# Optimization experiments

Hardware: AMD Instinct MI355X
Metric: run time of the kernel (lower is better)

The kernel has to match this reference:

```python
import jax, jax.numpy as jnp
import numpy as np

B, M = 512, 32          # graphs, atoms per graph
N = B * M               # 16384 nodes
F_IN, H, L = 16, 128, 2 # input feat, hidden, n interaction layers
CUTOFF = 1.0
BOX = 2.0               # side of position box -> avg degree ~16 at r=1


def _glorot(k, shape):
    fan_in = shape[-2]
    return jax.random.normal(k, shape, dtype=jnp.float32) / np.sqrt(fan_in)


def setup_inputs():
    key = jax.random.key(0)
    ks = jax.random.split(key, 12)
    return {
        "h": jax.random.normal(ks[0], (N, F_IN), dtype=jnp.float32),
        "x": jax.random.uniform(ks[1], (N, 3), dtype=jnp.float32) * BOX,
        "batch": jnp.repeat(jnp.arange(B, dtype=jnp.int32), M),
        "W_in": _glorot(ks[2], (F_IN, H)), "b_in": jnp.zeros((H,), jnp.float32),
        "We1": _glorot(ks[3], (L, 2 * H + 1, H)), "be1": jnp.zeros((L, H), jnp.float32),
        "We2": _glorot(ks[4], (L, H, H)), "be2": jnp.zeros((L, H), jnp.float32),
        "Wh1": _glorot(ks[5], (L, 2 * H, H)), "bh1": jnp.zeros((L, H), jnp.float32),
        "Wh2": _glorot(ks[6], (L, H, H)), "bh2": jnp.zeros((L, H), jnp.float32),
        "W_out": _glorot(ks[7], (H, H)), "b_out": jnp.zeros((H,), jnp.float32),
        "Wn1": _glorot(ks[8], (H, H)), "bn1": jnp.zeros((H,), jnp.float32),
        "Wn2": _glorot(ks[9], (H, 1)), "bn2": jnp.zeros((1,), jnp.float32),
    }


def reference(h, x, batch, W_in, b_in, We1, be1, We2, be2, Wh1, bh1, Wh2, bh2, W_out, b_out, Wn1, bn1, Wn2, bn2):
    # radius graph within each molecule, fixed-shape dense mask [B,M,M]
    xg = x.reshape(B, M, 3)
    diff = xg[:, :, None, :] - xg[:, None, :, :]                 # [B,M,M,3]
    d2 = jnp.sum(diff * diff, axis=-1)                            # [B,M,M]
    adj = (d2 < CUTOFF * CUTOFF) & (~jnp.eye(M, dtype=bool))      # no self-loops

    hg = (h @ W_in + b_in).reshape(B, M, H)                       # embedding_in
    for l in range(L):  # sake_conv interaction layers
        Wa, Wb, wd = We1[l, :H], We1[l, H:2 * H], We1[l, 2 * H]
        mi = jnp.einsum('bmh,hk->bmk', hg, Wa)
        mj = jnp.einsum('bmh,hk->bmk', hg, Wb)
        # edge message phi_e([h_i, h_j, ||x_i-x_j||^2])
        m = jax.nn.silu(mi[:, :, None, :] + mj[:, None, :, :] + d2[..., None] * wd + be1[l])
        m = jax.nn.silu(jnp.einsum('bijh,hk->bijk', m, We2[l]) + be2[l])
        m = jnp.where(adj[..., None], m, 0.0)
        agg = jnp.sum(m, axis=2)                                  # scatter-add over neighbors j
        # node update phi_h([h_i, m_i]) with residual
        u = jax.nn.silu(jnp.einsum('bmh,hk->bmk', hg, Wh1[l, :H])
                        + jnp.einsum('bmh,hk->bmk', agg, Wh1[l, H:]) + bh1[l])
        hg = hg + jnp.einsum('bmh,hk->bmk', u, Wh2[l]) + bh2[l]

    ho = hg.reshape(N, H) @ W_out + b_out                         # embedding_out
    e = jax.nn.silu(ho @ Wn1 + bn1) @ Wn2 + bn2                   # energy_network -> [N,1]
    out = jax.ops.segment_sum(e, batch, num_segments=B)           # per-graph energy pooling
    return out.squeeze()
```

## Files before the change

kernel.cpp:

```cpp
#include <hip/hip_runtime.h>
#include <hip/hip_bf16.h>


#define NB 512

typedef __bf16 bf16x8 __attribute__((ext_vector_type(8)));
typedef __bf16 bf16x2 __attribute__((ext_vector_type(2)));
typedef float f32x4 __attribute__((ext_vector_type(4)));

__device__ __forceinline__ unsigned short f2bf(float f) {
    unsigned int u = __float_as_uint(f);
    u = u + 0x7FFFu + ((u >> 16) & 1u);
    return (unsigned short)(u >> 16);
}
__device__ __forceinline__ unsigned int packbf(float lo, float hi) {
    bf16x2 t;
    t.x = (__bf16)lo;
    t.y = (__bf16)hi;
    return __builtin_bit_cast(unsigned int, t);
}
__device__ __forceinline__ float bflo(unsigned int u) { return __uint_as_float(u << 16); }
__device__ __forceinline__ float bfhi(unsigned int u) { return __uint_as_float(u & 0xffff0000u); }
__device__ __forceinline__ float bf2f(unsigned short u) { return __uint_as_float((unsigned int)u << 16); }
__device__ __forceinline__ float silu_f(float v) {
    return v * __builtin_amdgcn_rcpf(1.0f + __expf(-v));
}

__global__ __launch_bounds__(256) void prep_weights(
        const float* __restrict__ We1, const float* __restrict__ We2,
        const float* __restrict__ Wh1, const float* __restrict__ Wh2,
        const float* __restrict__ W_out, const float* __restrict__ Wn1,
        unsigned short* __restrict__ ws) {
    __shared__ unsigned short t[32][33];
    const int mtx  = blockIdx.x >> 4;
    const int tile = blockIdx.x & 15;
    const int kt = tile >> 2, nt = tile & 3;
    const int tx = threadIdx.x & 31, ty = threadIdx.x >> 5;

    const int l    = (mtx < 12) ? (mtx / 6) : 0;
    const int kind = (mtx < 12) ? (mtx % 6) : (6 + (mtx - 12));
    const float* src = nullptr;
    switch (kind) {
        case 0: src = We1 + (size_t)(l*257      )*128; break;
        case 1: src = We1 + (size_t)(l*257 + 128)*128; break;
        case 2: src = We2 + (size_t)(l*128      )*128; break;
        case 3: src = Wh1 + (size_t)(l*256      )*128; break;
        case 4: src = Wh1 + (size_t)(l*256 + 128)*128; break;
        case 5: src = Wh2 + (size_t)(l*128      )*128; break;
        case 6: src = W_out; break;
        case 7: src = Wn1;  break;
    }
    #pragma unroll
    for (int r = 0; r < 4; r++) {
        int k = kt*32 + ty + r*8;
        int n = nt*32 + tx;
        t[tx][ty + r*8] = f2bf(src[(size_t)k*128 + n]);
    }
    __syncthreads();
    unsigned short* dst = ws + ((size_t)mtx << 14);
    #pragma unroll
    for (int r = 0; r < 4; r++) {
        int nl = ty + r*8;
        int n = nt*32 + nl, k = kt*32 + tx;
        dst[(size_t)n*128 + k] = t[nl][tx];
    }
}

#define MFMA16(ACC, A, B) (ACC) = __builtin_amdgcn_mfma_f32_16x16x32_bf16((A), (B), (ACC), 0, 0, 0)

__global__ __launch_bounds__(256, 2) void sake_kernel(
    const float* __restrict__ h,   const float* __restrict__ x,
    const float* __restrict__ W_in,const float* __restrict__ b_in,
    const float* __restrict__ We1, const float* __restrict__ be1,
    const float* __restrict__ be2, const float* __restrict__ bh1,
    const float* __restrict__ bh2, const float* __restrict__ b_out,
    const float* __restrict__ bn1, const float* __restrict__ Wn2,
    const float* __restrict__ bn2, const unsigned short* __restrict__ wt,
    float* __restrict__ out)
{
    __shared__ __align__(16) float          s_hg[32*129];
    __shared__ __align__(16) unsigned short s_mimj[32*264];
    __shared__ __align__(16) unsigned short s_A1[32*136];
    __shared__ __align__(16) unsigned short s_A2[32*136];
    __shared__ __align__(16) float          s_nd2[32*16];
    __shared__ __align__(16) float          s_wd[128];
    __shared__ __align__(16) unsigned short s_be2[128];
    __shared__ __align__(16) unsigned char  s_nbr[32][16];
    __shared__ __align__(16) unsigned char  s_cnt[32];

    const int tid  = threadIdx.x;
    const int b    = blockIdx.x;
    const int w    = tid >> 6;
    const int lane = tid & 63;
    const int quad = lane >> 4;
    const int lm   = lane & 15;
    const int mt   = w & 1;
    const int ng   = w >> 1;

    if (tid < 32) {
        const float xx = x[(b*32+tid)*3+0];
        const float xy = x[(b*32+tid)*3+1];
        const float xz = x[(b*32+tid)*3+2];
        int c = 0;
        for (int j = 0; j < 32; j++) {
            float ox = __shfl(xx, j);
            float oy = __shfl(xy, j);
            float oz = __shfl(xz, j);
            float dx = xx - ox, dy = xy - oy, dz = xz - oz;
            float d2 = dx*dx + dy*dy + dz*dz;
            if (d2 < 1.0f && j != tid) {
                if (c < 16) { s_nbr[tid][c] = (unsigned char)j; s_nd2[tid*16 + c] = d2; }
                c++;
            }
        }
        for (int q = c; q < 16; q++) { s_nbr[tid][q] = (unsigned char)tid; s_nd2[tid*16 + q] = 0.0f; }
        s_cnt[tid] = (unsigned char)c;
    }
    {
        int k = tid & 127, mg = tid >> 7;
        float c0 = W_in[       k], c1 = W_in[ 128+k], c2 = W_in[ 256+k], c3 = W_in[ 384+k];
        float c4 = W_in[ 512+k], c5 = W_in[ 640+k], c6 = W_in[ 768+k], c7 = W_in[ 896+k];
        float c8 = W_in[1024+k], c9 = W_in[1152+k], c10= W_in[1280+k], c11= W_in[1408+k];
        float c12= W_in[1536+k], c13= W_in[1664+k], c14= W_in[1792+k], c15= W_in[1920+k];
        float bi = b_in[k];
        for (int rr = 0; rr < 16; rr++) {
            int m = mg*16 + rr;
            const float4* h4 = (const float4*)(h + (size_t)(b*32 + m)*16);
            float4 h0 = h4[0], h1 = h4[1], h2 = h4[2], h3 = h4[3];
            float acc = bi
                + h0.x*c0  + h0.y*c1  + h0.z*c2  + h0.w*c3
                + h1.x*c4  + h1.y*c5  + h1.z*c6  + h1.w*c7
                + h2.x*c8  + h2.y*c9  + h2.z*c10 + h2.w*c11
                + h3.x*c12 + h3.y*c13 + h3.z*c14 + h3.w*c15;
            s_hg[m*129 + k] = acc;
        }
    }
    __syncthreads();

    for (int l = 0; l < 2; l++) {
        {
            int m = tid >> 3, c = (tid & 7) * 16;
            const float* hp = &s_hg[m*129 + c];
            uint4 pa, pb;
            pa.x = packbf(hp[0],  hp[1]);  pa.y = packbf(hp[2],  hp[3]);
            pa.z = packbf(hp[4],  hp[5]);  pa.w = packbf(hp[6],  hp[7]);
            pb.x = packbf(hp[8],  hp[9]);  pb.y = packbf(hp[10], hp[11]);
            pb.z = packbf(hp[12], hp[13]); pb.w = packbf(hp[14], hp[15]);
            *(uint4*)&s_A1[m*136 + c]     = pa;
            *(uint4*)&s_A1[m*136 + c + 8] = pb;
        }
        if (tid < 128) {
            s_wd[tid]  = We1[(l*257 + 256)*128 + tid];
            s_be2[tid] = f2bf(be2[l*128 + tid]);
        }
        __syncthreads();

        #pragma unroll 1
        for (int t4 = 0; t4 < 8; t4++) {
            int nt = ng + t4*2;
            const unsigned short* bt = wt + (((size_t)l*6 + (nt < 8 ? 0 : 1)) << 14);
            int ncl = (nt & 7)*16 + lm;
            f32x4 acc = {0.f,0.f,0.f,0.f};
            #pragma unroll
            for (int kb = 0; kb < 4; kb++) {
                bf16x8 a  = *(const bf16x8*)&s_A1[(mt*16+lm)*136 + kb*32 + quad*8];
                bf16x8 bb = *(const bf16x8*)&bt[ncl*128 + kb*32 + quad*8];
                MFMA16(acc, a, bb);
            }
            int c = nt*16 + lm;
            float bias = (nt >= 8) ? be1[l*128 + ncl] : 0.0f;
            s_mimj[(mt*16 + quad*4 + 0)*264 + c] = f2bf(acc.x + bias);
            s_mimj[(mt*16 + quad*4 + 1)*264 + c] = f2bf(acc.y + bias);
            s_mimj[(mt*16 + quad*4 + 2)*264 + c] = f2bf(acc.z + bias);
            s_mimj[(mt*16 + quad*4 + 3)*264 + c] = f2bf(acc.w + bias);
        }
        __syncthreads();

        {
            const unsigned short* we2t = wt + (((size_t)l*6 + 2) << 14);
            const unsigned short* bbase = we2t + lm*128 + quad*8;
            bf16x8 b0 = *(const bf16x8*)(bbase      );
            bf16x8 b1 = *(const bf16x8*)(bbase +  32);
            bf16x8 b2 = *(const bf16x8*)(bbase +  64);
            bf16x8 b3 = *(const bf16x8*)(bbase +  96);
            #pragma unroll 1
            for (int ii = 0; ii < 8; ii++) {
                const int i = ii*4 + w;
                const int cnt = s_cnt[i];
                const uint4 miu0 = *(const uint4*)&s_mimj[i*264 +  0 + quad*8];
                const uint4 miu1 = *(const uint4*)&s_mimj[i*264 + 32 + quad*8];
                const uint4 miu2 = *(const uint4*)&s_mimj[i*264 + 64 + quad*8];
                const uint4 miu3 = *(const uint4*)&s_mimj[i*264 + 96 + quad*8];
#define MAKE_AF(J, KB, MIU, AF) { \
    const uint4 mju = *(const uint4*)&s_mimj[(J)*264 + 128 + (KB)*32 + quad*8]; \
    const float4 wa = *(const float4*)&s_wd[(KB)*32 + quad*8]; \
    const float4 wb = *(const float4*)&s_wd[(KB)*32 + quad*8 + 4]; \
    uint4 au; \
    au.x = packbf(silu_f(bflo(MIU.x)+bflo(mju.x)+d2v*wa.x), silu_f(bfhi(MIU.x)+bfhi(mju.x)+d2v*wa.y)); \
    au.y = packbf(silu_f(bflo(MIU.y)+bflo(mju.y)+d2v*wa.z), silu_f(bfhi(MIU.y)+bfhi(mju.y)+d2v*wa.w)); \
    au.z = packbf(silu_f(bflo(MIU.z)+bflo(mju.z)+d2v*wb.x), silu_f(bfhi(MIU.z)+bfhi(mju.z)+d2v*wb.y)); \
    au.w = packbf(silu_f(bflo(MIU.w)+bflo(mju.w)+d2v*wb.z), silu_f(bfhi(MIU.w)+bfhi(mju.w)+d2v*wb.w)); \
    AF = __builtin_bit_cast(bf16x8, au); }
                if (cnt <= 16) {
                    const int j = s_nbr[i][lm];
                    const float d2v = s_nd2[i*16 + lm];
                    bf16x8 a00, a01, a02, a03;
                    MAKE_AF(j, 0, miu0, a00) MAKE_AF(j, 1, miu1, a01)
                    MAKE_AF(j, 2, miu2, a02) MAKE_AF(j, 3, miu3, a03)
                    const int jb0 = quad*4;
                    const float mk00 = (jb0 + 0 < cnt) ? 1.f : 0.f;
                    const float mk01 = (jb0 + 1 < cnt) ? 1.f : 0.f;
                    const float mk02 = (jb0 + 2 < cnt) ? 1.f : 0.f;
                    const float mk03 = (jb0 + 3 < cnt) ? 1.f : 0.f;
                    #pragma unroll 1
                    for (int nt = 0; nt < 8; nt++) {
                        const unsigned short* np = bbase + (((nt + 1) & 7) * 2048);
                        bf16x8 n0 = *(const bf16x8*)(np      );
                        bf16x8 n1 = *(const bf16x8*)(np +  32);
                        bf16x8 n2 = *(const bf16x8*)(np +  64);
                        bf16x8 n3 = *(const bf16x8*)(np +  96);
                        f32x4 ac0 = {0.f,0.f,0.f,0.f};
                        MFMA16(ac0, a00, b0); MFMA16(ac0, a01, b1);
                        MFMA16(ac0, a02, b2); MFMA16(ac0, a03, b3);
                        const float bv = bf2f(s_be2[nt*16 + lm]);
                        float part = mk00*silu_f(ac0.x + bv) + mk01*silu_f(ac0.y + bv)
                                   + mk02*silu_f(ac0.z + bv) + mk03*silu_f(ac0.w + bv);
                        part += __shfl_xor(part, 16);
                        part += __shfl_xor(part, 32);
                        if (lane < 16) s_A2[i*136 + nt*16 + lane] = f2bf(part);
                        b0 = n0; b1 = n1; b2 = n2; b3 = n3;
                    }
                } else {
                    const float xi0 = x[(b*32+i)*3+0];
                    const float xi1 = x[(b*32+i)*3+1];
                    const float xi2 = x[(b*32+i)*3+2];
                    float da0 = xi0 - x[(b*32+lm)*3+0];
                    float da1 = xi1 - x[(b*32+lm)*3+1];
                    float da2 = xi2 - x[(b*32+lm)*3+2];
                    const float d2a = da0*da0 + da1*da1 + da2*da2;
                    float db0 = xi0 - x[(b*32+16+lm)*3+0];
                    float db1 = xi1 - x[(b*32+16+lm)*3+1];
                    float db2 = xi2 - x[(b*32+16+lm)*3+2];
                    const float d2b = db0*db0 + db1*db1 + db2*db2;
                    const unsigned long long balA = __ballot(d2a < 1.0f && lm != i);
                    const unsigned long long balB = __ballot(d2b < 1.0f && (16+lm) != i);
                    bf16x8 a00, a01, a02, a03;
                    bf16x8 a10, a11, a12, a13;
                    {
                        const int j = lm;
                        const float d2v = d2a;
                        MAKE_AF(j, 0, miu0, a00) MAKE_AF(j, 1, miu1, a01)
                        MAKE_AF(j, 2, miu2, a02) MAKE_AF(j, 3, miu3, a03)
                    }
                    {
                        const int j = 16 + lm;
                        const float d2v = d2b;
                        MAKE_AF(j, 0, miu0, a10) MAKE_AF(j, 1, miu1, a11)
                        MAKE_AF(j, 2, miu2, a12) MAKE_AF(j, 3, miu3, a13)
                    }
                    const int jb0 = quad*4;
                    const float mk00 = ((balA >> (jb0 + 0)) & 1ull) ? 1.f : 0.f;
                    const float mk01 = ((balA >> (jb0 + 1)) & 1ull) ? 1.f : 0.f;
                    const float mk02 = ((balA >> (jb0 + 2)) & 1ull) ? 1.f : 0.f;
                    const float mk03 = ((balA >> (jb0 + 3)) & 1ull) ? 1.f : 0.f;
                    const float mk10 = ((balB >> (jb0 + 0)) & 1ull) ? 1.f : 0.f;
                    const float mk11 = ((balB >> (jb0 + 1)) & 1ull) ? 1.f : 0.f;
                    const float mk12 = ((balB >> (jb0 + 2)) & 1ull) ? 1.f : 0.f;
                    const float mk13 = ((balB >> (jb0 + 3)) & 1ull) ? 1.f : 0.f;
                    #pragma unroll 1
                    for (int nt = 0; nt < 8; nt++) {
                        const unsigned short* np = bbase + (((nt + 1) & 7) * 2048);
                        bf16x8 n0 = *(const bf16x8*)(np      );
                        bf16x8 n1 = *(const bf16x8*)(np +  32);
                        bf16x8 n2 = *(const bf16x8*)(np +  64);
                        bf16x8 n3 = *(const bf16x8*)(np +  96);
                        f32x4 ac0 = {0.f,0.f,0.f,0.f};
                        f32x4 ac1 = {0.f,0.f,0.f,0.f};
                        MFMA16(ac0, a00, b0); MFMA16(ac0, a01, b1);
                        MFMA16(ac0, a02, b2); MFMA16(ac0, a03, b3);
                        MFMA16(ac1, a10, b0); MFMA16(ac1, a11, b1);
                        MFMA16(ac1, a12, b2); MFMA16(ac1, a13, b3);
                        const float bv = bf2f(s_be2[nt*16 + lm]);
                        float part = mk00*silu_f(ac0.x + bv) + mk01*silu_f(ac0.y + bv)
                                   + mk02*silu_f(ac0.z + bv) + mk03*silu_f(ac0.w + bv)
                                   + mk10*silu_f(ac1.x + bv) + mk11*silu_f(ac1.y + bv)
                                   + mk12*silu_f(ac1.z + bv) + mk13*silu_f(ac1.w + bv);
                        part += __shfl_xor(part, 16);
                        part += __shfl_xor(part, 32);
                        if (lane < 16) s_A2[i*136 + nt*16 + lane] = f2bf(part);
                        b0 = n0; b1 = n1; b2 = n2; b3 = n3;
                    }
                }
#undef MAKE_AF
            }
        }
        __syncthreads();

        unsigned short* s_u = s_mimj;
        {
            const unsigned short* w1a = wt + (((size_t)l*6 + 3) << 14);
            const unsigned short* w1b = wt + (((size_t)l*6 + 4) << 14);
#define U_GEMM(T2) { \
    const int nt = ng + (T2)*2, ncl = nt*16 + lm; \
    f32x4 acc = {0.f,0.f,0.f,0.f}; \
    _Pragma("unroll") \
    for (int kb = 0; kb < 4; kb++) { \
        bf16x8 a  = *(const bf16x8*)&s_A1[(mt*16+lm)*136 + kb*32 + quad*8]; \
        bf16x8 bb = *(const bf16x8*)&w1a[ncl*128 + kb*32 + quad*8]; \
        MFMA16(acc, a, bb); } \
    _Pragma("unroll") \
    for (int kb = 0; kb < 4; kb++) { \
        bf16x8 a  = *(const bf16x8*)&s_A2[(mt*16+lm)*136 + kb*32 + quad*8]; \
        bf16x8 bb = *(const bf16x8*)&w1b[ncl*128 + kb*32 + quad*8]; \
        MFMA16(acc, a, bb); } \
    const float bh = bh1[l*128 + ncl]; \
    s_u[(mt*16 + quad*4 + 0)*136 + ncl] = f2bf(silu_f(acc.x + bh)); \
    s_u[(mt*16 + quad*4 + 1)*136 + ncl] = f2bf(silu_f(acc.y + bh)); \
    s_u[(mt*16 + quad*4 + 2)*136 + ncl] = f2bf(silu_f(acc.z + bh)); \
    s_u[(mt*16 + quad*4 + 3)*136 + ncl] = f2bf(silu_f(acc.w + bh)); }
            U_GEMM(0) U_GEMM(1) U_GEMM(2) U_GEMM(3)
#undef U_GEMM
        }
        __syncthreads();

        {
            const unsigned short* w2 = wt + (((size_t)l*6 + 5) << 14);
#define H_GEMM(T2) { \
    const int nt = ng + (T2)*2, ncl = nt*16 + lm; \
    f32x4 acc = {0.f,0.f,0.f,0.f}; \
    _Pragma("unroll") \
    for (int kb = 0; kb < 4; kb++) { \
        bf16x8 a  = *(const bf16x8*)&s_u[(mt*16+lm)*136 + kb*32 + quad*8]; \
        bf16x8 bb = *(const bf16x8*)&w2[ncl*128 + kb*32 + quad*8]; \
        MFMA16(acc, a, bb); } \
    const float bh = bh2[l*128 + ncl]; \
    s_hg[(mt*16 + quad*4 + 0)*129 + ncl] += acc.x + bh; \
    s_hg[(mt*16 + quad*4 + 1)*129 + ncl] += acc.y + bh; \
    s_hg[(mt*16 + quad*4 + 2)*129 + ncl] += acc.z + bh; \
    s_hg[(mt*16 + quad*4 + 3)*129 + ncl] += acc.w + bh; }
            H_GEMM(0) H_GEMM(1) H_GEMM(2) H_GEMM(3)
#undef H_GEMM
        }
        __syncthreads();
    }

    {
        int m = tid >> 3, c = (tid & 7) * 16;
        const float* hp = &s_hg[m*129 + c];
        uint4 pa, pb;
        pa.x = packbf(hp[0],  hp[1]);  pa.y = packbf(hp[2],  hp[3]);
        pa.z = packbf(hp[4],  hp[5]);  pa.w = packbf(hp[6],  hp[7]);
        pb.x = packbf(hp[8],  hp[9]);  pb.y = packbf(hp[10], hp[11]);
        pb.z = packbf(hp[12], hp[13]); pb.w = packbf(hp[14], hp[15]);
        *(uint4*)&s_A1[m*136 + c]     = pa;
        *(uint4*)&s_A1[m*136 + c + 8] = pb;
    }
    __syncthreads();
    {
        const unsigned short* wo = wt + ((size_t)12 << 14);
#define O_GEMM(T2) { \
    const int nt = ng + (T2)*2, ncl = nt*16 + lm; \
    f32x4 acc = {0.f,0.f,0.f,0.f}; \
    _Pragma("unroll") \
    for (int kb = 0; kb < 4; kb++) { \
        bf16x8 a  = *(const bf16x8*)&s_A1[(mt*16+lm)*136 + kb*32 + quad*8]; \
        bf16x8 bb = *(const bf16x8*)&wo[ncl*128 + kb*32 + quad*8]; \
        MFMA16(acc, a, bb); } \
    const float bo = b_out[ncl]; \
    s_A2[(mt*16 + quad*4 + 0)*136 + ncl] = f2bf(acc.x + bo); \
    s_A2[(mt*16 + quad*4 + 1)*136 + ncl] = f2bf(acc.y + bo); \
    s_A2[(mt*16 + quad*4 + 2)*136 + ncl] = f2bf(acc.z + bo); \
    s_A2[(mt*16 + quad*4 + 3)*136 + ncl] = f2bf(acc.w + bo); }
        O_GEMM(0) O_GEMM(1) O_GEMM(2) O_GEMM(3)
#undef O_GEMM
    }
    __syncthreads();
    float* s_g = (float*)s_mimj;
    {
        const unsigned short* wn1 = wt + ((size_t)13 << 14);
#define G_GEMM(T2) { \
    const int nt = ng + (T2)*2, ncl = nt*16 + lm; \
    f32x4 acc = {0.f,0.f,0.f,0.f}; \
    _Pragma("unroll") \
    for (int kb = 0; kb < 4; kb++) { \
        bf16x8 a  = *(const bf16x8*)&s_A2[(mt*16+lm)*136 + kb*32 + quad*8]; \
        bf16x8 bb = *(const bf16x8*)&wn1[ncl*128 + kb*32 + quad*8]; \
        MFMA16(acc, a, bb); } \
    const float bn = bn1[ncl]; \
    s_g[(mt*16 + quad*4 + 0)*129 + ncl] = silu_f(acc.x + bn); \
    s_g[(mt*16 + quad*4 + 1)*129 + ncl] = silu_f(acc.y + bn); \
    s_g[(mt*16 + quad*4 + 2)*129 + ncl] = silu_f(acc.z + bn); \
    s_g[(mt*16 + quad*4 + 3)*129 + ncl] = silu_f(acc.w + bn); }
        G_GEMM(0) G_GEMM(1) G_GEMM(2) G_GEMM(3)
#undef G_GEMM
    }
    __syncthreads();
    float* s_ep = s_nd2;
    {
        int m = tid >> 3, s = tid & 7;
        float acc = 0.f;
        #pragma unroll
        for (int q = 0; q < 16; q++) {
            int hh = s*16 + q;
            acc += s_g[m*129 + hh] * Wn2[hh];
        }
        s_ep[tid] = acc;
    }
    __syncthreads();
    if (tid < 32) {
        float e = bn2[0];
        #pragma unroll
        for (int s = 0; s < 8; s++) e += s_ep[tid*8 + s];
        #pragma unroll
        for (int off = 16; off >= 1; off >>= 1) e += __shfl_down(e, off, 32);
        if (tid == 0) out[b] = e;
    }
}

extern "C" void kernel_launch(void* const* d_in, const int* in_sizes, int n_in,
                              void* d_out, int out_size, void* d_ws, size_t ws_size,
                              hipStream_t stream) {
    const float* h     = (const float*)d_in[0];
    const float* x     = (const float*)d_in[1];
    const float* W_in  = (const float*)d_in[3];
    const float* b_in  = (const float*)d_in[4];
    const float* We1   = (const float*)d_in[5];
    const float* be1   = (const float*)d_in[6];
    const float* We2   = (const float*)d_in[7];
    const float* be2   = (const float*)d_in[8];
    const float* Wh1   = (const float*)d_in[9];
    const float* bh1   = (const float*)d_in[10];
    const float* Wh2   = (const float*)d_in[11];
    const float* bh2   = (const float*)d_in[12];
    const float* W_out = (const float*)d_in[13];
    const float* b_out = (const float*)d_in[14];
    const float* Wn1   = (const float*)d_in[15];
    const float* bn1   = (const float*)d_in[16];
    const float* Wn2   = (const float*)d_in[17];
    const float* bn2   = (const float*)d_in[18];
    unsigned short* ws = (unsigned short*)d_ws;
    float* outp = (float*)d_out;

    prep_weights<<<14*16, 256, 0, stream>>>(We1, We2, Wh1, Wh2, W_out, Wn1, ws);
    sake_kernel<<<NB, 256, 0, stream>>>(h, x, W_in, b_in, We1, be1, be2, bh1, bh2,
                                        b_out, bn1, Wn2, bn2, ws, outp);
}
```

Measured before the change: 256.9 us.

## Hold full We2 tile in registers and fuse bf16 staging into producer stages

The edge-MLP second GEMM now preloads all eight We2 column tiles (32 bf16x8 vectors) and the be2 bias values into registers once per layer. The nt loop is fully unrolled, so it no longer reloads weights from global memory for every node i. The bf16 copy of hg in s_A1 is now written directly by the embedding and residual-update stages. This removes the separate pack passes and two barriers per layer, and the mi/mj GEMM loop is unrolled by two. The cost is much higher register pressure, which could lower occupancy or cause spills.

Measured after the change: 218.0 us. -15.1%, faster.

```diff
diff --git a/kernel.cpp b/kernel.cpp
--- a/kernel.cpp
+++ b/kernel.cpp
@@ -133,29 +133,18 @@
                 + h2.x*c8  + h2.y*c9  + h2.z*c10 + h2.w*c11
                 + h3.x*c12 + h3.y*c13 + h3.z*c14 + h3.w*c15;
             s_hg[m*129 + k] = acc;
+            s_A1[m*136 + k] = f2bf(acc);
         }
     }
     __syncthreads();
 
     for (int l = 0; l < 2; l++) {
-        {
-            int m = tid >> 3, c = (tid & 7) * 16;
-            const float* hp = &s_hg[m*129 + c];
-            uint4 pa, pb;
-            pa.x = packbf(hp[0],  hp[1]);  pa.y = packbf(hp[2],  hp[3]);
-            pa.z = packbf(hp[4],  hp[5]);  pa.w = packbf(hp[6],  hp[7]);
-            pb.x = packbf(hp[8],  hp[9]);  pb.y = packbf(hp[10], hp[11]);
-            pb.z = packbf(hp[12], hp[13]); pb.w = packbf(hp[14], hp[15]);
-            *(uint4*)&s_A1[m*136 + c]     = pa;
-            *(uint4*)&s_A1[m*136 + c + 8] = pb;
-        }
         if (tid < 128) {
             s_wd[tid]  = We1[(l*257 + 256)*128 + tid];
             s_be2[tid] = f2bf(be2[l*128 + tid]);
         }
-        __syncthreads();
-
-        #pragma unroll 1
+
+        #pragma unroll 2
         for (int t4 = 0; t4 < 8; t4++) {
             int nt = ng + t4*2;
             const unsigned short* bt = wt + (((size_t)l*6 + (nt < 8 ? 0 : 1)) << 14);
@@ -179,10 +168,17 @@
         {
             const unsigned short* we2t = wt + (((size_t)l*6 + 2) << 14);
             const unsigned short* bbase = we2t + lm*128 + quad*8;
-            bf16x8 b0 = *(const bf16x8*)(bbase      );
-            bf16x8 b1 = *(const bf16x8*)(bbase +  32);
-            bf16x8 b2 = *(const bf16x8*)(bbase +  64);
-            bf16x8 b3 = *(const bf16x8*)(bbase +  96);
+            bf16x8 wreg[8][4];
+            #pragma unroll
+            for (int nt = 0; nt < 8; nt++) {
+                #pragma unroll
+                for (int kb = 0; kb < 4; kb++)
+                    wreg[nt][kb] = *(const bf16x8*)(bbase + nt*2048 + kb*32);
+            }
+            float bvv[8];
+            #pragma unroll
+            for (int nt = 0; nt < 8; nt++) bvv[nt] = bf2f(s_be2[nt*16 + lm]);
+
             #pragma unroll 1
             for (int ii = 0; ii < 8; ii++) {
                 const int i = ii*4 + w;
@@ -212,23 +208,17 @@
                     const float mk01 = (jb0 + 1 < cnt) ? 1.f : 0.f;
                     const float mk02 = (jb0 + 2 < cnt) ? 1.f : 0.f;
                     const float mk03 = (jb0 + 3 < cnt) ? 1.f : 0.f;
-                    #pragma unroll 1
+                    #pragma unroll
                     for (int nt = 0; nt < 8; nt++) {
-                        const unsigned short* np = bbase + (((nt + 1) & 7) * 2048);
-                        bf16x8 n0 = *(const bf16x8*)(np      );
-                        bf16x8 n1 = *(const bf16x8*)(np +  32);
-                        bf16x8 n2 = *(const bf16x8*)(np +  64);
-                        bf16x8 n3 = *(const bf16x8*)(np +  96);
                         f32x4 ac0 = {0.f,0.f,0.f,0.f};
-                        MFMA16(ac0, a00, b0); MFMA16(ac0, a01, b1);
-                        MFMA16(ac0, a02, b2); MFMA16(ac0, a03, b3);
-                        const float bv = bf2f(s_be2[nt*16 + lm]);
+                        MFMA16(ac0, a00, wreg[nt][0]); MFMA16(ac0, a01, wreg[nt][1]);
+                        MFMA16(ac0, a02, wreg[nt][2]); MFMA16(ac0, a03, wreg[nt][3]);
+                        const float bv = bvv[nt];
                         float part = mk00*silu_f(ac0.x + bv) + mk01*silu_f(ac0.y + bv)
                                    + mk02*silu_f(ac0.z + bv) + mk03*silu_f(ac0.w + bv);
                         part += __shfl_xor(part, 16);
                         part += __shfl_xor(part, 32);
                         if (lane < 16) s_A2[i*136 + nt*16 + lane] = f2bf(part);
-                        b0 = n0; b1 = n1; b2 = n2; b3 = n3;
                     }
                 } else {
                     const float xi0 = x[(b*32+i)*3+0];
@@ -267,20 +257,15 @@
                     const float mk11 = ((balB >> (jb0 + 1)) & 1ull) ? 1.f : 0.f;
                     const float mk12 = ((balB >> (jb0 + 2)) & 1ull) ? 1.f : 0.f;
                     const float mk13 = ((balB >> (jb0 + 3)) & 1ull) ? 1.f : 0.f;
-                    #pragma unroll 1
+                    #pragma unroll
                     for (int nt = 0; nt < 8; nt++) {
-                        const unsigned short* np = bbase + (((nt + 1) & 7) * 2048);
-                        bf16x8 n0 = *(const bf16x8*)(np      );
-                        bf16x8 n1 = *(const bf16x8*)(np +  32);
-                        bf16x8 n2 = *(const bf16x8*)(np +  64);
-                        bf16x8 n3 = *(const bf16x8*)(np +  96);
                         f32x4 ac0 = {0.f,0.f,0.f,0.f};
                         f32x4 ac1 = {0.f,0.f,0.f,0.f};
-                        MFMA16(ac0, a00, b0); MFMA16(ac0, a01, b1);
-                        MFMA16(ac0, a02, b2); MFMA16(ac0, a03, b3);
-                        MFMA16(ac1, a10, b0); MFMA16(ac1, a11, b1);
-                        MFMA16(ac1, a12, b2); MFMA16(ac1, a13, b3);
-                        const float bv = bf2f(s_be2[nt*16 + lm]);
+                        MFMA16(ac0, a00, wreg[nt][0]); MFMA16(ac0, a01, wreg[nt][1]);
+                        MFMA16(ac0, a02, wreg[nt][2]); MFMA16(ac0, a03, wreg[nt][3]);
+                        MFMA16(ac1, a10, wreg[nt][0]); MFMA16(ac1, a11, wreg[nt][1]);
+                        MFMA16(ac1, a12, wreg[nt][2]); MFMA16(ac1, a13, wreg[nt][3]);
+                        const float bv = bvv[nt];
                         float part = mk00*silu_f(ac0.x + bv) + mk01*silu_f(ac0.y + bv)
                                    + mk02*silu_f(ac0.z + bv) + mk03*silu_f(ac0.w + bv)
                                    + mk10*silu_f(ac1.x + bv) + mk11*silu_f(ac1.y + bv)
@@ -288,7 +273,6 @@
                         part += __shfl_xor(part, 16);
                         part += __shfl_xor(part, 32);
                         if (lane < 16) s_A2[i*136 + nt*16 + lane] = f2bf(part);
-                        b0 = n0; b1 = n1; b2 = n2; b3 = n3;
                     }
                 }
 #undef MAKE_AF
@@ -334,28 +318,20 @@
         bf16x8 bb = *(const bf16x8*)&w2[ncl*128 + kb*32 + quad*8]; \
         MFMA16(acc, a, bb); } \
     const float bh = bh2[l*128 + ncl]; \
-    s_hg[(mt*16 + quad*4 + 0)*129 + ncl] += acc.x + bh; \
-    s_hg[(mt*16 + quad*4 + 1)*129 + ncl] += acc.y + bh; \
-    s_hg[(mt*16 + quad*4 + 2)*129 + ncl] += acc.z + bh; \
-    s_hg[(mt*16 + quad*4 + 3)*129 + ncl] += acc.w + bh; }
+    { float v = s_hg[(mt*16 + quad*4 + 0)*129 + ncl] + acc.x + bh; \
+      s_hg[(mt*16 + quad*4 + 0)*129 + ncl] = v; s_A1[(mt*16 + quad*4 + 0)*136 + ncl] = f2bf(v); } \
+    { float v = s_hg[(mt*16 + quad*4 + 1)*129 + ncl] + acc.y + bh; \
+      s_hg[(mt*16 + quad*4 + 1)*129 + ncl] = v; s_A1[(mt*16 + quad*4 + 1)*136 + ncl] = f2bf(v); } \
+    { float v = s_hg[(mt*16 + quad*4 + 2)*129 + ncl] + acc.z + bh; \
+      s_hg[(mt*16 + quad*4 + 2)*129 + ncl] = v; s_A1[(mt*16 + quad*4 + 2)*136 + ncl] = f2bf(v); } \
+    { float v = s_hg[(mt*16 + quad*4 + 3)*129 + ncl] + acc.w + bh; \
+      s_hg[(mt*16 + quad*4 + 3)*129 + ncl] = v; s_A1[(mt*16 + quad*4 + 3)*136 + ncl] = f2bf(v); } }
             H_GEMM(0) H_GEMM(1) H_GEMM(2) H_GEMM(3)
 #undef H_GEMM
         }
         __syncthreads();
     }
 
-    {
-        int m = tid >> 3, c = (tid & 7) * 16;
-        const float* hp = &s_hg[m*129 + c];
-        uint4 pa, pb;
-        pa.x = packbf(hp[0],  hp[1]);  pa.y = packbf(hp[2],  hp[3]);
-        pa.z = packbf(hp[4],  hp[5]);  pa.w = packbf(hp[6],  hp[7]);
-        pb.x = packbf(hp[8],  hp[9]);  pb.y = packbf(hp[10], hp[11]);
-        pb.z = packbf(hp[12], hp[13]); pb.w = packbf(hp[14], hp[15]);
-        *(uint4*)&s_A1[m*136 + c]     = pa;
-        *(uint4*)&s_A1[m*136 + c + 8] = pb;
-    }
-    __syncthreads();
     {
         const unsigned short* wo = wt + ((size_t)12 << 14);
 #define O_GEMM(T2) { \
```
